# Kernel tuning notes

Hardware: AMD Instinct MI355X
Metric: run time of the kernel (lower is better)

## Reference

```python
import jax, jax.numpy as jnp
import numpy as np

B, C, H, W = 8, 21, 512, 512
MAX_M = 0.5   # args.ldam_max_m
S = 30.0      # args.ldam_s


def setup_inputs() -> dict:
    key = jax.random.key(0)
    k1, k2 = jax.random.split(key)
    pred = jax.random.normal(k1, (B, C, H, W), dtype=jnp.float32)
    target = jax.random.randint(k2, (B, H, W), 0, C, dtype=jnp.int32)  # class labels (argmax of one-hot)
    return {"pred": pred, "target": target}


def reference(pred, target):
    labels = target.reshape(-1)  # [N]
    # m_list: per-class pixel counts == sum of one-hot target over (0,2,3)
    counts = jnp.zeros((C,), dtype=pred.dtype).at[labels].add(1.0)
    m_list = 1.0 / jnp.sqrt(jnp.sqrt(counts + 1e-4))
    m_list = m_list * (MAX_M / jnp.max(m_list))

    logits = pred.transpose(0, 2, 3, 1).reshape(-1, C)  # [N, C]
    batch_m = m_list[labels]                            # gather == matmul(m_list, one_hot^T)
    onehot = jax.nn.one_hot(labels, C, dtype=logits.dtype)
    output = logits - batch_m[:, None] * onehot         # subtract margin only at target class

    logp = jax.nn.log_softmax(S * output, axis=-1)
    nll = -jnp.take_along_axis(logp, labels[:, None].astype(jnp.int32), axis=1)[:, 0]
    return jnp.mean(nll)
```

## Files before the change

### kernel.cpp

```cpp
#include <hip/hip_runtime.h>

static constexpr int   Bn  = 8;
static constexpr int   Cc  = 21;
static constexpr int   Hh  = 512;
static constexpr int   Ww  = 512;
static constexpr int   HWn = Hh * Ww;
static constexpr int   Nn  = Bn * HWn;
static constexpr float MAXM = 0.5f;
static constexpr float Sc   = 30.0f;

static constexpr int WS_COUNTS = 0;
static constexpr int WS_ACC    = 96;
static constexpr int WS_SM     = 128;

__global__ __launch_bounds__(256) void hist_kernel(const int4* __restrict__ t4,
                                                   int* __restrict__ counts) {
    __shared__ int lh[Cc];
    int t = threadIdx.x;
    if (t < Cc) lh[t] = 0;
    __syncthreads();
    int tid = blockIdx.x * 256 + t;
    int4 v = t4[tid];
    atomicAdd(&lh[v.x], 1);
    atomicAdd(&lh[v.y], 1);
    atomicAdd(&lh[v.z], 1);
    atomicAdd(&lh[v.w], 1);
    __syncthreads();
    if (t < Cc) atomicAdd(&counts[t], lh[t]);
}

__global__ __launch_bounds__(64) void mlist_kernel(const int* __restrict__ counts,
                                                   float* __restrict__ sm) {
    int t = threadIdx.x;
    float mval = 0.0f;
    if (t < Cc) {
        float cnt = (float)counts[t] + 1e-4f;
        mval = 1.0f / sqrtf(sqrtf(cnt));
    }
    float mx = mval;
    #pragma unroll
    for (int o = 32; o >= 1; o >>= 1) mx = fmaxf(mx, __shfl_down(mx, o));
    mx = __shfl(mx, 0);
    if (t < Cc) sm[t] = Sc * mval * (MAXM / mx);
}

__global__ __launch_bounds__(256) void loss_kernel(const float* __restrict__ pred,
                                                   const int4* __restrict__ t4,
                                                   const float* __restrict__ smg,
                                                   double* __restrict__ acc) {
    __shared__ float s_sm[Cc];
    int t = threadIdx.x;
    if (t < Cc) s_sm[t] = smg[t];
    __syncthreads();

    int tid = blockIdx.x * 256 + t;
    int n0  = tid * 4;
    int b   = n0 >> 18;
    int hw  = n0 & (HWn - 1);
    const float4* p4 = (const float4*)(pred + (size_t)b * Cc * HWn + hw);

    int4 y4 = t4[tid];
    int ys[4] = {y4.x, y4.y, y4.z, y4.w};
    float smy[4];
    #pragma unroll
    for (int k = 0; k < 4; ++k) smy[k] = s_sm[ys[k]];

    float v[Cc][4];
    float mx[4] = {-1e30f, -1e30f, -1e30f, -1e30f};
    float vy[4] = {0.f, 0.f, 0.f, 0.f};

    #pragma unroll
    for (int c = 0; c < Cc; ++c) {
        float4 x = p4[(size_t)c * (HWn / 4)];
        float xs[4] = {x.x, x.y, x.z, x.w};
        #pragma unroll
        for (int k = 0; k < 4; ++k) {
            float val = Sc * xs[k] - (c == ys[k] ? smy[k] : 0.0f);
            v[c][k] = val;
            mx[k] = fmaxf(mx[k], val);
            if (c == ys[k]) vy[k] = val;
        }
    }

    float nll = 0.0f;
    #pragma unroll
    for (int k = 0; k < 4; ++k) {
        float sum = 0.0f;
        #pragma unroll
        for (int c = 0; c < Cc; ++c) sum += __expf(v[c][k] - mx[k]);
        nll += __logf(sum) + mx[k] - vy[k];
    }

    #pragma unroll
    for (int o = 32; o >= 1; o >>= 1) nll += __shfl_down(nll, o);

    __shared__ float wsum[4];
    int wave = t >> 6;
    int lane = t & 63;
    if (lane == 0) wsum[wave] = nll;
    __syncthreads();
    if (t == 0) {
        float bsum = wsum[0] + wsum[1] + wsum[2] + wsum[3];
        atomicAdd(acc, (double)bsum);
    }
}

__global__ void final_kernel(const double* __restrict__ acc, float* __restrict__ out) {
    out[0] = (float)(acc[0] / (double)Nn);
}

extern "C" void kernel_launch(void* const* d_in, const int* in_sizes, int n_in,
                              void* d_out, int out_size, void* d_ws, size_t ws_size,
                              hipStream_t stream) {
    const float* pred   = (const float*)d_in[0];
    const int*   target = (const int*)d_in[1];
    float*       out    = (float*)d_out;

    char* ws = (char*)d_ws;
    int*    counts = (int*)(ws + WS_COUNTS);
    double* acc    = (double*)(ws + WS_ACC);
    float*  sm     = (float*)(ws + WS_SM);

    hipMemsetAsync(d_ws, 0, 256, stream);

    const int nvec   = Nn / 4;
    const int blocks = nvec / 256;

    hist_kernel <<<blocks, 256, 0, stream>>>((const int4*)target, counts);
    mlist_kernel<<<1,       64, 0, stream>>>(counts, sm);
    loss_kernel <<<blocks, 256, 0, stream>>>(pred, (const int4*)target, sm, acc);
    final_kernel<<<1,        1, 0, stream>>>(acc, out);
}
```

Before: 274.0 us.

## Fuse m_list and final kernels into loss kernel, use online softmax

Drops the single-block m_list kernel and the final division kernel. Each loss block now computes the class margins and their maximum directly from the histogram counts, and the last block to finish writes the mean using a done counter. The log-softmax becomes a single-pass online max-and-sum, so the 84-value register array is gone. This cuts two launches and lowers register pressure, but adds extra exp calls per element and a redundant per-block margin computation.

```diff
diff --git a/kernel.cpp b/kernel.cpp
--- a/kernel.cpp
+++ b/kernel.cpp
@@ -1,17 +1,14 @@
 #include <hip/hip_runtime.h>
 
-static constexpr int   Bn  = 8;
 static constexpr int   Cc  = 21;
-static constexpr int   Hh  = 512;
-static constexpr int   Ww  = 512;
-static constexpr int   HWn = Hh * Ww;
-static constexpr int   Nn  = Bn * HWn;
+static constexpr int   HWn = 512 * 512;
+static constexpr int   Nn  = 8 * HWn;
 static constexpr float MAXM = 0.5f;
 static constexpr float Sc   = 30.0f;
 
 static constexpr int WS_COUNTS = 0;
 static constexpr int WS_ACC    = 96;
-static constexpr int WS_SM     = 128;
+static constexpr int WS_DONE   = 104;
 
 __global__ __launch_bounds__(256) void hist_kernel(const int4* __restrict__ t4,
                                                    int* __restrict__ counts) {
@@ -29,29 +26,23 @@
     if (t < Cc) atomicAdd(&counts[t], lh[t]);
 }
 
-__global__ __launch_bounds__(64) void mlist_kernel(const int* __restrict__ counts,
-                                                   float* __restrict__ sm) {
-    int t = threadIdx.x;
-    float mval = 0.0f;
-    if (t < Cc) {
-        float cnt = (float)counts[t] + 1e-4f;
-        mval = 1.0f / sqrtf(sqrtf(cnt));
-    }
-    float mx = mval;
-    #pragma unroll
-    for (int o = 32; o >= 1; o >>= 1) mx = fmaxf(mx, __shfl_down(mx, o));
-    mx = __shfl(mx, 0);
-    if (t < Cc) sm[t] = Sc * mval * (MAXM / mx);
-}
-
 __global__ __launch_bounds__(256) void loss_kernel(const float* __restrict__ pred,
                                                    const int4* __restrict__ t4,
-                                                   const float* __restrict__ smg,
-                                                   double* __restrict__ acc) {
+                                                   const int* __restrict__ counts,
+                                                   double* __restrict__ acc,
+                                                   int* __restrict__ done,
+                                                   float* __restrict__ out) {
     __shared__ float s_sm[Cc];
+    __shared__ float wsum[4];
+
     int t = threadIdx.x;
-    if (t < Cc) s_sm[t] = smg[t];
+    if (t < Cc) s_sm[t] = 1.0f / sqrtf(sqrtf((float)counts[t] + 1e-4f));
     __syncthreads();
+
+    float mxm = s_sm[0];
+    #pragma unroll
+    for (int i = 1; i < Cc; ++i) mxm = fmaxf(mxm, s_sm[i]);
+    float scl = Sc * (MAXM / mxm);
 
     int tid = blockIdx.x * 256 + t;
     int n0  = tid * 4;
@@ -63,10 +54,10 @@
     int ys[4] = {y4.x, y4.y, y4.z, y4.w};
     float smy[4];
     #pragma unroll
-    for (int k = 0; k < 4; ++k) smy[k] = s_sm[ys[k]];
+    for (int k = 0; k < 4; ++k) smy[k] = s_sm[ys[k]] * scl;
 
-    float v[Cc][4];
-    float mx[4] = {-1e30f, -1e30f, -1e30f, -1e30f};
+    float m[4]  = {-1e30f, -1e30f, -1e30f, -1e30f};
+    float su[4] = {0.f, 0.f, 0.f, 0.f};
     float vy[4] = {0.f, 0.f, 0.f, 0.f};
 
     #pragma unroll
@@ -75,26 +66,22 @@
         float xs[4] = {x.x, x.y, x.z, x.w};
         #pragma unroll
         for (int k = 0; k < 4; ++k) {
-            float val = Sc * xs[k] - (c == ys[k] ? smy[k] : 0.0f);
-            v[c][k] = val;
-            mx[k] = fmaxf(mx[k], val);
-            if (c == ys[k]) vy[k] = val;
+            bool  isy = (c == ys[k]);
+            float val = fmaf(Sc, xs[k], isy ? -smy[k] : 0.0f);
+            vy[k] = isy ? val : vy[k];
+            float nm = fmaxf(m[k], val);
+            su[k] = su[k] * __expf(m[k] - nm) + __expf(val - nm);
+            m[k] = nm;
         }
     }
 
     float nll = 0.0f;
     #pragma unroll
-    for (int k = 0; k < 4; ++k) {
-        float sum = 0.0f;
-        #pragma unroll
-        for (int c = 0; c < Cc; ++c) sum += __expf(v[c][k] - mx[k]);
-        nll += __logf(sum) + mx[k] - vy[k];
-    }
+    for (int k = 0; k < 4; ++k) nll += __logf(su[k]) + m[k] - vy[k];
 
     #pragma unroll
     for (int o = 32; o >= 1; o >>= 1) nll += __shfl_down(nll, o);
 
-    __shared__ float wsum[4];
     int wave = t >> 6;
     int lane = t & 63;
     if (lane == 0) wsum[wave] = nll;
@@ -102,11 +89,14 @@
     if (t == 0) {
         float bsum = wsum[0] + wsum[1] + wsum[2] + wsum[3];
         atomicAdd(acc, (double)bsum);
+        __threadfence();
+        int prev = atomicAdd(done, 1);
+        if (prev == (int)gridDim.x - 1) {
+            __threadfence();
+            double total = atomicAdd(acc, 0.0);
+            out[0] = (float)(total / (double)Nn);
+        }
     }
-}
-
-__global__ void final_kernel(const double* __restrict__ acc, float* __restrict__ out) {
-    out[0] = (float)(acc[0] / (double)Nn);
 }
 
 extern "C" void kernel_launch(void* const* d_in, const int* in_sizes, int n_in,
@@ -119,15 +109,14 @@
     char* ws = (char*)d_ws;
     int*    counts = (int*)(ws + WS_COUNTS);
     double* acc    = (double*)(ws + WS_ACC);
-    float*  sm     = (float*)(ws + WS_SM);
+    int*    done   = (int*)(ws + WS_DONE);
 
     hipMemsetAsync(d_ws, 0, 256, stream);
 
     const int nvec   = Nn / 4;
     const int blocks = nvec / 256;
 
-    hist_kernel <<<blocks, 256, 0, stream>>>((const int4*)target, counts);
-    mlist_kernel<<<1,       64, 0, stream>>>(counts, sm);
-    loss_kernel <<<blocks, 256, 0, stream>>>(pred, (const int4*)target, sm, acc);
-    final_kernel<<<1,        1, 0, stream>>>(acc, out);
+    hist_kernel<<<blocks, 256, 0, stream>>>((const int4*)target, counts);
+    loss_kernel<<<blocks, 256, 0, stream>>>(pred, (const int4*)target, counts,
+                                            acc, done, out);
 }
```

Result: slower. 360.2 us (+31.4%).
